# Kernel optimization log

Measured on AMD Instinct MI355X. Metric: run time of the kernel, lower is better.

## Reference

```python
import jax, jax.numpy as jnp
import numpy as np

N_HEADS = 8
D_MODEL = 512
HEAD_DIM = D_MODEL // N_HEADS


def setup_inputs() -> dict:
    key = jax.random.key(0)
    ks = jax.random.split(key, 9)
    B, T1, T2, D = 1, 4096, 4096, D_MODEL
    w_scale = 0.02
    return {
        "query": jax.random.normal(ks[0], (B, T1, D), dtype=jnp.float32),
        "key": jax.random.normal(ks[1], (B, T2, D), dtype=jnp.float32),
        "value": jax.random.normal(ks[2], (B, T2, D), dtype=jnp.float32),
        # True = padded (masked out); ~half positions masked
        "key_padding_mask": jax.random.randint(ks[3], (B, T2), 0, 2) == 1,
        "Wq_w": jax.random.normal(ks[4], (D, D), dtype=jnp.float32) * w_scale,
        "Wq_b": jnp.zeros((D,), dtype=jnp.float32),
        "Wk_w": jax.random.normal(ks[5], (D, D), dtype=jnp.float32) * w_scale,
        "Wk_b": jnp.zeros((D,), dtype=jnp.float32),
        "Wv_w": jax.random.normal(ks[6], (D, D), dtype=jnp.float32) * w_scale,
        "Wv_b": jnp.zeros((D,), dtype=jnp.float32),
        "Wo_w": jax.random.normal(ks[7], (D, D), dtype=jnp.float32) * w_scale,
        "Wo_b": jnp.zeros((D,), dtype=jnp.float32),
    }


def reference(query, key, value, key_padding_mask,
              Wq_w, Wq_b, Wk_w, Wk_b, Wv_w, Wv_b, Wo_w, Wo_b):
    B, T1, D = query.shape
    T2 = key.shape[1]
    H, HD = N_HEADS, HEAD_DIM

    # torch Linear: y = x @ W.T + b
    q = (query @ Wq_w.T + Wq_b).reshape(B, T1, H, HD).transpose(0, 2, 1, 3)  # [B,H,T1,HD]
    k = (key @ Wk_w.T + Wk_b).reshape(B, T2, H, HD).transpose(0, 2, 1, 3)    # [B,H,T2,HD]
    v = (value @ Wv_w.T + Wv_b).reshape(B, T2, H, HD).transpose(0, 2, 1, 3)  # [B,H,T2,HD]

    scale = 1.0 / (HD ** 0.5)
    scores = jnp.einsum("bhqd,bhkd->bhqk", q, k) * scale                     # [B,H,T1,T2]
    mask_value = jnp.finfo(scores.dtype).min
    scores = jnp.where(key_padding_mask[:, None, None, :], mask_value, scores)

    attn = jax.nn.softmax(scores, axis=-1)                                   # [B,H,T1,T2]
    # dropout p=0.0 (inference) -> identity

    out = jnp.einsum("bhqk,bhkd->bhqd", attn, v)                             # [B,H,T1,HD]
    out = out.transpose(0, 2, 1, 3).reshape(B, T1, D)
    out = out @ Wo_w.T + Wo_b
    return (out, attn)
```

## Files before the change

kernel.cpp:

```cpp
#include <hip/hip_runtime.h>
#include <hip/hip_bf16.h>
#include <float.h>
#include <stdint.h>

typedef __bf16 bf16x8 __attribute__((ext_vector_type(8)));
typedef __bf16 bf16x4 __attribute__((ext_vector_type(4)));
typedef float  f32x4  __attribute__((ext_vector_type(4)));

#define T_SEQ 4096
#define DMODEL 512
#define NH 8
#define HDIM 64
#define KS1 4
#define L2E 1.44269504088896340736f

__device__ __forceinline__ float fexp2(float x) { return __builtin_amdgcn_exp2f(x); }

__device__ __forceinline__ void gl_lds16(const __bf16* g, char* l) {
    __builtin_amdgcn_global_load_lds(
        (const __attribute__((address_space(1))) unsigned int*)(g),
        (__attribute__((address_space(3))) unsigned int*)(l),
        16, 0, 0);
}

__global__ __launch_bounds__(256) void qkv_kernel(
    const float* __restrict__ qin, const float* __restrict__ kin, const float* __restrict__ vin,
    const float* __restrict__ Wq, const float* __restrict__ bq,
    const float* __restrict__ Wk, const float* __restrict__ bk,
    const float* __restrict__ Wv, const float* __restrict__ bv,
    __bf16* __restrict__ qo, __bf16* __restrict__ ko, __bf16* __restrict__ vt)
{
    __shared__ char lds[16384];
    char* Ab = lds;
    char* Bb = lds + 8192;

    const int z = blockIdx.z;
    const float* X    = (z == 0) ? qin : (z == 1) ? kin : vin;
    const float* W    = (z == 0) ? Wq  : (z == 1) ? Wk  : Wv;
    const float* bias = (z == 0) ? bq  : (z == 1) ? bk  : bv;

    const int m0 = blockIdx.x * 64;
    const int n0 = blockIdx.y * 64;
    const int tid  = threadIdx.x;
    const int w    = tid >> 6;
    const int lane = tid & 63;
    const int lrow = lane & 15;
    const int lgrp = lane >> 4;

    f32x4 acc[4] = {};
    const int r  = tid >> 2;
    const int c0 = (tid & 3) * 16;

    for (int kt = 0; kt < 8; ++kt) {
        const int k0 = kt * 64;
        const float* gA = X + (size_t)(m0 + r) * DMODEL + k0 + c0;
        const float* gB = W + (size_t)(n0 + r) * DMODEL + k0 + c0;
        const int sw = (r & 7) << 4;
#pragma unroll
        for (int i = 0; i < 4; ++i) {
            float4 a4 = *(const float4*)(gA + 4 * i);
            float4 b4 = *(const float4*)(gB + 4 * i);
            bf16x4 av, bv4;
            av[0] = (__bf16)a4.x; av[1] = (__bf16)a4.y; av[2] = (__bf16)a4.z; av[3] = (__bf16)a4.w;
            bv4[0] = (__bf16)b4.x; bv4[1] = (__bf16)b4.y; bv4[2] = (__bf16)b4.z; bv4[3] = (__bf16)b4.w;
            *(bf16x4*)(Ab + r * 128 + ((c0 * 2 + 8 * i) ^ sw)) = av;
            *(bf16x4*)(Bb + r * 128 + ((c0 * 2 + 8 * i) ^ sw)) = bv4;
        }
        __syncthreads();
#pragma unroll
        for (int ks = 0; ks < 2; ++ks) {
            bf16x8 af = *(const bf16x8*)(Ab + (w * 16 + lrow) * 128 +
                                         ((ks * 64 + lgrp * 16) ^ ((lrow & 7) << 4)));
#pragma unroll
            for (int ns = 0; ns < 4; ++ns) {
                bf16x8 bf = *(const bf16x8*)(Bb + (ns * 16 + lrow) * 128 +
                                             ((ks * 64 + lgrp * 16) ^ ((lrow & 7) << 4)));
                acc[ns] = __builtin_amdgcn_mfma_f32_16x16x32_bf16(af, bf, acc[ns], 0, 0, 0);
            }
        }
        __syncthreads();
    }

    if (z == 2) {
        char* LT = lds;
#pragma unroll
        for (int ns = 0; ns < 4; ++ns) {
            float bcol = bias[n0 + ns * 16 + lrow];
#pragma unroll
            for (int rr = 0; rr < 4; ++rr) {
                int col = ns * 16 + lrow;
                int row = w * 16 + lgrp * 4 + rr;
                *(__bf16*)(LT + col * 128 + ((row * 2) ^ ((col & 7) << 4))) =
                    (__bf16)(acc[ns][rr] + bcol);
            }
        }
        __syncthreads();
        int d  = tid >> 2;
        int nb = (tid & 3) * 32;
        bf16x8 t0 = *(const bf16x8*)(LT + d * 128 + (nb ^ ((d & 7) << 4)));
        bf16x8 t1 = *(const bf16x8*)(LT + d * 128 + ((nb + 16) ^ ((d & 7) << 4)));
        __bf16* dst = vt + (size_t)(n0 + d) * T_SEQ + m0 + (tid & 3) * 16;
        *(bf16x8*)dst = t0;
        *(bf16x8*)(dst + 8) = t1;
    } else {
        __bf16* out = (z == 0) ? qo : ko;
        const float sc = (z == 0) ? 0.125f : 1.0f;
#pragma unroll
        for (int ns = 0; ns < 4; ++ns) {
            float bcol = bias[n0 + ns * 16 + lrow];
#pragma unroll
            for (int rr = 0; rr < 4; ++rr) {
                int orow = m0 + w * 16 + lgrp * 4 + rr;
                out[(size_t)orow * DMODEL + n0 + ns * 16 + lrow] =
                    (__bf16)((acc[ns][rr] + bcol) * sc);
            }
        }
    }
}

__global__ __launch_bounds__(256) void attn_stats(
    const __bf16* __restrict__ qb, const __bf16* __restrict__ kb,
    const int* __restrict__ mask, float* __restrict__ l_part)
{
    __shared__ char lds[16384];
    char* KB0 = lds;
    char* KB1 = lds + 8192;

    const int nwg  = 32 * NH * KS1;
    const int b    = blockIdx.x;
    const int rmap = (b & 7) * (nwg >> 3) + (b >> 3);
    const int qsi  = rmap & 31;
    const int h    = (rmap >> 5) & (NH - 1);
    const int ksp  = rmap >> 8;
    const int q0   = qsi * 128;
    const int k0   = ksp * (T_SEQ / KS1);

    const int tid  = threadIdx.x;
    const int w    = tid >> 6;
    const int lane = tid & 63;
    const int lrow = lane & 15;
    const int lgrp = lane >> 4;
    const int swl  = (lrow & 7) << 4;
    const int q0w  = q0 + w * 32;

    bf16x8 qa[2][2];
#pragma unroll
    for (int q2 = 0; q2 < 2; ++q2) {
        const __bf16* qp = qb + (size_t)(q0w + q2 * 16 + lrow) * DMODEL + h * HDIM;
        qa[q2][0] = *(const bf16x8*)(qp + lgrp * 8);
        qa[q2][1] = *(const bf16x8*)(qp + 32 + lgrp * 8);
    }

    const int key0 = w * 16 + (lane >> 3);
    const int key1 = key0 + 8;
    const int g    = lane & 7;
    const __bf16* sK0 = kb + (size_t)(k0 + key0) * DMODEL + h * HDIM + (g ^ (key0 & 7)) * 8;
    const __bf16* sK1 = kb + (size_t)(k0 + key1) * DMODEL + h * HDIM + (g ^ (key1 & 7)) * 8;

    float lsum[2][4] = {};

    gl_lds16(sK0, KB0 + w * 2048);
    gl_lds16(sK1, KB0 + w * 2048 + 1024);
    __syncthreads();

    char* cur = KB0;
    char* nxt = KB1;
    const int NT = (T_SEQ / KS1) / 64;
    for (int kt = 0; kt < NT; ++kt) {
        if (kt + 1 < NT) {
            gl_lds16(sK0 + (size_t)(kt + 1) * 64 * DMODEL, nxt + w * 2048);
            gl_lds16(sK1 + (size_t)(kt + 1) * 64 * DMODEL, nxt + w * 2048 + 1024);
        }

        f32x4 acc[2][4] = {};
        __builtin_amdgcn_s_setprio(1);
#pragma unroll
        for (int ns = 0; ns < 4; ++ns) {
            bf16x8 kf0 = *(const bf16x8*)(cur + (ns * 16 + lrow) * 128 + ((lgrp * 16) ^ swl));
            bf16x8 kf1 = *(const bf16x8*)(cur + (ns * 16 + lrow) * 128 + ((64 + lgrp * 16) ^ swl));
            acc[0][ns] = __builtin_amdgcn_mfma_f32_16x16x32_bf16(kf0, qa[0][0], acc[0][ns], 0, 0, 0);
            acc[0][ns] = __builtin_amdgcn_mfma_f32_16x16x32_bf16(kf1, qa[0][1], acc[0][ns], 0, 0, 0);
            acc[1][ns] = __builtin_amdgcn_mfma_f32_16x16x32_bf16(kf0, qa[1][0], acc[1][ns], 0, 0, 0);
            acc[1][ns] = __builtin_amdgcn_mfma_f32_16x16x32_bf16(kf1, qa[1][1], acc[1][ns], 0, 0, 0);
        }
        __builtin_amdgcn_s_setprio(0);

#pragma unroll
        for (int ns = 0; ns < 4; ++ns) {
            int4 mi = *(const int4*)(mask + k0 + kt * 64 + ns * 16 + lgrp * 4);
            f32x4 mb;
            mb[0] = mi.x ? -1e30f : 0.f;
            mb[1] = mi.y ? -1e30f : 0.f;
            mb[2] = mi.z ? -1e30f : 0.f;
            mb[3] = mi.w ? -1e30f : 0.f;
#pragma unroll
            for (int q2 = 0; q2 < 2; ++q2)
#pragma unroll
                for (int rr = 0; rr < 4; ++rr)
                    lsum[q2][ns] += fexp2(fmaf(acc[q2][ns][rr], L2E, mb[rr]));
        }
        __syncthreads();
        char* t = cur; cur = nxt; nxt = t;
    }

#pragma unroll
    for (int q2 = 0; q2 < 2; ++q2) {
        float tot = (lsum[q2][0] + lsum[q2][1]) + (lsum[q2][2] + lsum[q2][3]);
        tot += __shfl_xor(tot, 16);
        tot += __shfl_xor(tot, 32);
        if (lgrp == 0)
            l_part[((size_t)h * KS1 + ksp) * T_SEQ + q0w + q2 * 16 + lrow] = tot;
    }
}

__global__ __launch_bounds__(256) void attn_main(
    const __bf16* __restrict__ qb, const __bf16* __restrict__ kb,
    const __bf16* __restrict__ vt, const int* __restrict__ mask,
    const float* __restrict__ l_part,
    float* __restrict__ attn_out, void* __restrict__ opart,
    int KSP2, int of32)
{
    __shared__ char lds[40960];
    char* PB  = lds + 32768;

    const int nwg  = 64 * NH * KSP2;
    const int b    = blockIdx.x;
    const int rmap = (b & 7) * (nwg >> 3) + (b >> 3);
    const int qbi  = rmap & 63;
    const int h    = (rmap >> 6) & (NH - 1);
    const int kz   = rmap >> 9;
    const int q0   = qbi * 64;
    const int kspan = T_SEQ / KSP2;
    const int k0   = kz * kspan;
    const int NT   = kspan / 64;

    const int tid  = threadIdx.x;
    const int w    = tid >> 6;
    const int lane = tid & 63;
    const int lrow = lane & 15;
    const int lgrp = lane >> 4;
    const int swl  = (lrow & 7) << 4;

    bf16x8 qa[2];
    {
        const __bf16* qp = qb + (size_t)(q0 + w * 16 + lrow) * DMODEL + h * HDIM;
        qa[0] = *(const bf16x8*)(qp + lgrp * 8);
        qa[1] = *(const bf16x8*)(qp + 32 + lgrp * 8);
    }

    float rl;
    {
        float s = 0.f;
#pragma unroll
        for (int ks = 0; ks < KS1; ++ks)
            s += l_part[((size_t)h * KS1 + ks) * T_SEQ + q0 + w * 16 + lrow];
        rl = 1.0f / s;
    }

    const int key0 = w * 16 + (lane >> 3);
    const int key1 = key0 + 8;
    const int g    = lane & 7;
    const __bf16* sK0 = kb + (size_t)(k0 + key0) * DMODEL + h * HDIM + (g ^ (key0 & 7)) * 8;
    const __bf16* sK1 = kb + (size_t)(k0 + key1) * DMODEL + h * HDIM + (g ^ (key1 & 7)) * 8;
    const __bf16* sV0 = vt + (size_t)(h * HDIM + key0) * T_SEQ + k0 + (g ^ (key0 & 7)) * 8;
    const __bf16* sV1 = vt + (size_t)(h * HDIM + key1) * T_SEQ + k0 + (g ^ (key1 & 7)) * 8;

#define STAGE(tt, buf) do {                                             \
        size_t koff_ = (size_t)(tt) * 64 * DMODEL;                      \
        size_t voff_ = (size_t)(tt) * 64;                               \
        gl_lds16(sK0 + koff_, (buf) + w * 2048);                        \
        gl_lds16(sK1 + koff_, (buf) + w * 2048 + 1024);                 \
        gl_lds16(sV0 + voff_, (buf) + 8192 + w * 2048);                 \
        gl_lds16(sV1 + voff_, (buf) + 8192 + w * 2048 + 1024);          \
    } while (0)

    f32x4 oacc[4] = {};
    float* arow = attn_out + (size_t)h * T_SEQ * T_SEQ +
                  (size_t)(q0 + w * 16 + lrow) * T_SEQ + k0 + lgrp * 4;
    char* Pw = PB + w * 2048;

    char* bA = lds;
    char* bB = lds + 16384;

    STAGE(0, bA);
    __syncthreads();

    for (int kt = 0; kt < NT; ++kt) {
        if (kt + 1 < NT) STAGE(kt + 1, bB);

        f32x4 acc[4] = {};
        __builtin_amdgcn_s_setprio(1);
#pragma unroll
        for (int ns = 0; ns < 4; ++ns) {
            bf16x8 kf0 = *(const bf16x8*)(bA + (ns * 16 + lrow) * 128 + ((lgrp * 16) ^ swl));
            bf16x8 kf1 = *(const bf16x8*)(bA + (ns * 16 + lrow) * 128 + ((64 + lgrp * 16) ^ swl));
            acc[ns] = __builtin_amdgcn_mfma_f32_16x16x32_bf16(kf0, qa[0], acc[ns], 0, 0, 0);
            acc[ns] = __builtin_amdgcn_mfma_f32_16x16x32_bf16(kf1, qa[1], acc[ns], 0, 0, 0);
        }
        __builtin_amdgcn_s_setprio(0);

        f32x4 pvs[4];
#pragma unroll
        for (int ns = 0; ns < 4; ++ns) {
            int4 mi = *(const int4*)(mask + k0 + kt * 64 + ns * 16 + lgrp * 4);
            f32x4 mb;
            mb[0] = mi.x ? -1e30f : 0.f;
            mb[1] = mi.y ? -1e30f : 0.f;
            mb[2] = mi.z ? -1e30f : 0.f;
            mb[3] = mi.w ? -1e30f : 0.f;
            f32x4 pv;
#pragma unroll
            for (int rr = 0; rr < 4; ++rr)
                pv[rr] = fexp2(fmaf(acc[ns][rr], L2E, mb[rr])) * rl;
            pvs[ns] = pv;
            bf16x4 pb;
            pb[0] = (__bf16)pv[0]; pb[1] = (__bf16)pv[1];
            pb[2] = (__bf16)pv[2]; pb[3] = (__bf16)pv[3];
            *(bf16x4*)(Pw + lrow * 128 + ((ns * 32 + lgrp * 8) ^ swl)) = pb;
        }

        __builtin_amdgcn_s_setprio(1);
#pragma unroll
        for (int ks = 0; ks < 2; ++ks) {
            bf16x8 pa = *(const bf16x8*)(Pw + lrow * 128 + ((ks * 64 + lgrp * 16) ^ swl));
#pragma unroll
            for (int dsb = 0; dsb < 4; ++dsb) {
                bf16x8 vf = *(const bf16x8*)(bA + 8192 + (dsb * 16 + lrow) * 128 +
                                             ((ks * 64 + lgrp * 16) ^ swl));
                oacc[dsb] = __builtin_amdgcn_mfma_f32_16x16x32_bf16(vf, pa, oacc[dsb], 0, 0, 0);
            }
        }
        __builtin_amdgcn_s_setprio(0);

#pragma unroll
        for (int ns = 0; ns < 4; ++ns)
            *(f32x4*)(arow + kt * 64 + ns * 16) = pvs[ns];

        __syncthreads();
        char* tmp = bA; bA = bB; bB = tmp;
    }
#undef STAGE

    if (of32) {
        float* op = (float*)opart + (size_t)kz * T_SEQ * DMODEL +
                    (size_t)(q0 + w * 16 + lrow) * DMODEL + h * HDIM + lgrp * 4;
#pragma unroll
        for (int dsb = 0; dsb < 4; ++dsb)
            *(f32x4*)(op + dsb * 16) = oacc[dsb];
    } else {
        __bf16* op = (__bf16*)opart + (size_t)(q0 + w * 16 + lrow) * DMODEL + h * HDIM + lgrp * 4;
#pragma unroll
        for (int dsb = 0; dsb < 4; ++dsb) {
            bf16x4 ob;
            ob[0] = (__bf16)oacc[dsb][0]; ob[1] = (__bf16)oacc[dsb][1];
            ob[2] = (__bf16)oacc[dsb][2]; ob[3] = (__bf16)oacc[dsb][3];
            *(bf16x4*)(op + dsb * 16) = ob;
        }
    }
}

__global__ __launch_bounds__(256) void oproj_kernel(
    const void* __restrict__ opart, const float* __restrict__ Wo,
    const float* __restrict__ bo, float* __restrict__ out, int KSP2, int of32)
{
    __shared__ char lds[16384];
    char* Ab = lds;
    char* Bb = lds + 8192;

    const int m0 = blockIdx.x * 64;
    const int n0 = blockIdx.y * 64;
    const int tid  = threadIdx.x;
    const int w    = tid >> 6;
    const int lane = tid & 63;
    const int lrow = lane & 15;
    const int lgrp = lane >> 4;

    f32x4 acc[4] = {};
    const int r   = tid >> 2;
    const int c0e = (tid & 3) * 16;
    const int sw  = (r & 7) << 4;

    for (int kt = 0; kt < 8; ++kt) {
        const int k0 = kt * 64;
        if (of32) {
            const float* p0 = (const float*)opart + (size_t)(m0 + r) * DMODEL + k0 + c0e;
#pragma unroll
            for (int i = 0; i < 4; ++i) {
                f32x4 a4 = *(const f32x4*)(p0 + 4 * i);
                for (int s = 1; s < KSP2; ++s)
                    a4 = a4 + *(const f32x4*)(p0 + (size_t)s * T_SEQ * DMODEL + 4 * i);
                bf16x4 av;
                av[0] = (__bf16)a4[0]; av[1] = (__bf16)a4[1];
                av[2] = (__bf16)a4[2]; av[3] = (__bf16)a4[3];
                *(bf16x4*)(Ab + r * 128 + ((c0e * 2 + 8 * i) ^ sw)) = av;
            }
        } else {
            const __bf16* pa = (const __bf16*)opart + (size_t)(m0 + r) * DMODEL + k0 + c0e;
            bf16x8 a0 = *(const bf16x8*)pa;
            bf16x8 a1 = *(const bf16x8*)(pa + 8);
            *(bf16x8*)(Ab + r * 128 + ((c0e * 2) ^ sw)) = a0;
            *(bf16x8*)(Ab + r * 128 + ((c0e * 2 + 16) ^ sw)) = a1;
        }
        const float* gB = Wo + (size_t)(n0 + r) * DMODEL + k0 + c0e;
#pragma unroll
        for (int i = 0; i < 4; ++i) {
            float4 b4 = *(const float4*)(gB + 4 * i);
            bf16x4 bv4;
            bv4[0] = (__bf16)b4.x; bv4[1] = (__bf16)b4.y;
            bv4[2] = (__bf16)b4.z; bv4[3] = (__bf16)b4.w;
            *(bf16x4*)(Bb + r * 128 + ((c0e * 2 + 8 * i) ^ sw)) = bv4;
        }
        __syncthreads();
#pragma unroll
        for (int ks = 0; ks < 2; ++ks) {
            bf16x8 af = *(const bf16x8*)(Ab + (w * 16 + lrow) * 128 +
                                         ((ks * 64 + lgrp * 16) ^ ((lrow & 7) << 4)));
#pragma unroll
            for (int ns = 0; ns < 4; ++ns) {
                bf16x8 bf = *(const bf16x8*)(Bb + (ns * 16 + lrow) * 128 +
                                             ((ks * 64 + lgrp * 16) ^ ((lrow & 7) << 4)));
                acc[ns] = __builtin_amdgcn_mfma_f32_16x16x32_bf16(af, bf, acc[ns], 0, 0, 0);
            }
        }
        __syncthreads();
    }

#pragma unroll
    for (int ns = 0; ns < 4; ++ns) {
        float bcol = bo[n0 + ns * 16 + lrow];
#pragma unroll
        for (int rr = 0; rr < 4; ++rr) {
            int orow = m0 + w * 16 + lgrp * 4 + rr;
            out[(size_t)orow * DMODEL + n0 + ns * 16 + lrow] = acc[ns][rr] + bcol;
        }
    }
}

extern "C" void kernel_launch(void* const* d_in, const int* in_sizes, int n_in,
                              void* d_out, int out_size, void* d_ws, size_t ws_size,
                              hipStream_t stream) {
    const float* query = (const float*)d_in[0];
    const float* key   = (const float*)d_in[1];
    const float* value = (const float*)d_in[2];
    const int*   mask  = (const int*)d_in[3];
    const float* Wq = (const float*)d_in[4];
    const float* bq = (const float*)d_in[5];
    const float* Wk = (const float*)d_in[6];
    const float* bk = (const float*)d_in[7];
    const float* Wv = (const float*)d_in[8];
    const float* bv = (const float*)d_in[9];
    const float* Wo = (const float*)d_in[10];
    const float* bo = (const float*)d_in[11];

    float* out  = (float*)d_out;
    float* attn = out + (size_t)T_SEQ * DMODEL;

    char* ws = (char*)d_ws;
    __bf16* qo     = (__bf16*)(ws);
    __bf16* ko     = (__bf16*)(ws + (4u << 20));
    __bf16* vt     = (__bf16*)(ws + (8u << 20));
    float*  l_part = (float*)(ws + (12u << 20));
    void*   opart  = (void*)(ws + (12u << 20) + (1u << 19));
    const size_t obase = (12u << 20) + (1u << 19);

    int KSP2, of32;
    const size_t oslice = (size_t)T_SEQ * DMODEL * 4;
    if (ws_size >= obase + 2 * oslice)      { KSP2 = 2; of32 = 1; }
    else if (ws_size >= obase + oslice)     { KSP2 = 1; of32 = 1; }
    else                                    { KSP2 = 1; of32 = 0; }

    qkv_kernel<<<dim3(64, 8, 3), 256, 0, stream>>>(query, key, value,
                                                   Wq, bq, Wk, bk, Wv, bv, qo, ko, vt);
    attn_stats<<<dim3(32 * NH * KS1), 256, 0, stream>>>(qo, ko, mask, l_part);
    attn_main<<<dim3(64 * NH * KSP2), 256, 0, stream>>>(qo, ko, vt, mask, l_part,
                                                        attn, opart, KSP2, of32);
    oproj_kernel<<<dim3(64, 8), 256, 0, stream>>>(opart, Wo, bo, out, KSP2, of32);
}
```

Before: 233.5 us.

## Load V fragments directly from global into registers instead of via LDS

Removes V staging through LDS: each wave now loads its V^T MFMA fragments directly from global memory into registers, in two halves issued before and after the QK MFMAs. LDS shrinks from 40KB to 24KB, which may raise occupancy, and the attention-probability stores move into the softmax loop to save registers. The cost is that all four waves now redundantly fetch the same V tile from global or L2 with no cross-wave sharing, and the load latency is no longer hidden by the async double-buffered prefetch.

After: 288.7 us. 1.24x slower.

```diff
diff --git a/kernel.cpp b/kernel.cpp
--- a/kernel.cpp
+++ b/kernel.cpp
@@ -220,8 +220,8 @@
     float* __restrict__ attn_out, void* __restrict__ opart,
     int KSP2, int of32)
 {
-    __shared__ char lds[40960];
-    char* PB  = lds + 32768;
+    __shared__ char lds[24576];
+    char* PB  = lds + 16384;
 
     const int nwg  = 64 * NH * KSP2;
     const int b    = blockIdx.x;
@@ -262,16 +262,13 @@
     const int g    = lane & 7;
     const __bf16* sK0 = kb + (size_t)(k0 + key0) * DMODEL + h * HDIM + (g ^ (key0 & 7)) * 8;
     const __bf16* sK1 = kb + (size_t)(k0 + key1) * DMODEL + h * HDIM + (g ^ (key1 & 7)) * 8;
-    const __bf16* sV0 = vt + (size_t)(h * HDIM + key0) * T_SEQ + k0 + (g ^ (key0 & 7)) * 8;
-    const __bf16* sV1 = vt + (size_t)(h * HDIM + key1) * T_SEQ + k0 + (g ^ (key1 & 7)) * 8;
+
+    const __bf16* vbase = vt + (size_t)(h * HDIM + lrow) * T_SEQ + k0 + lgrp * 8;
 
 #define STAGE(tt, buf) do {                                             \
         size_t koff_ = (size_t)(tt) * 64 * DMODEL;                      \
-        size_t voff_ = (size_t)(tt) * 64;                               \
         gl_lds16(sK0 + koff_, (buf) + w * 2048);                        \
         gl_lds16(sK1 + koff_, (buf) + w * 2048 + 1024);                 \
-        gl_lds16(sV0 + voff_, (buf) + 8192 + w * 2048);                 \
-        gl_lds16(sV1 + voff_, (buf) + 8192 + w * 2048 + 1024);          \
     } while (0)
 
     f32x4 oacc[4] = {};
@@ -280,13 +277,19 @@
     char* Pw = PB + w * 2048;
 
     char* bA = lds;
-    char* bB = lds + 16384;
+    char* bB = lds + 8192;
 
     STAGE(0, bA);
     __syncthreads();
 
     for (int kt = 0; kt < NT; ++kt) {
         if (kt + 1 < NT) STAGE(kt + 1, bB);
+
+        const __bf16* vpt = vbase + (size_t)kt * 64;
+        bf16x8 vf0[4];
+#pragma unroll
+        for (int dsb = 0; dsb < 4; ++dsb)
+            vf0[dsb] = *(const bf16x8*)(vpt + (size_t)(dsb * 16) * T_SEQ);
 
         f32x4 acc[4] = {};
         __builtin_amdgcn_s_setprio(1);
@@ -299,7 +302,11 @@
         }
         __builtin_amdgcn_s_setprio(0);
 
-        f32x4 pvs[4];
+        bf16x8 vf1[4];
+#pragma unroll
+        for (int dsb = 0; dsb < 4; ++dsb)
+            vf1[dsb] = *(const bf16x8*)(vpt + (size_t)(dsb * 16) * T_SEQ + 32);
+
 #pragma unroll
         for (int ns = 0; ns < 4; ++ns) {
             int4 mi = *(const int4*)(mask + k0 + kt * 64 + ns * 16 + lgrp * 4);
@@ -312,29 +319,25 @@
 #pragma unroll
             for (int rr = 0; rr < 4; ++rr)
                 pv[rr] = fexp2(fmaf(acc[ns][rr], L2E, mb[rr])) * rl;
-            pvs[ns] = pv;
             bf16x4 pb;
             pb[0] = (__bf16)pv[0]; pb[1] = (__bf16)pv[1];
             pb[2] = (__bf16)pv[2]; pb[3] = (__bf16)pv[3];
             *(bf16x4*)(Pw + lrow * 128 + ((ns * 32 + lgrp * 8) ^ swl)) = pb;
+            *(f32x4*)(arow + kt * 64 + ns * 16) = pv;
         }
 
         __builtin_amdgcn_s_setprio(1);
-#pragma unroll
-        for (int ks = 0; ks < 2; ++ks) {
-            bf16x8 pa = *(const bf16x8*)(Pw + lrow * 128 + ((ks * 64 + lgrp * 16) ^ swl));
-#pragma unroll
-            for (int dsb = 0; dsb < 4; ++dsb) {
-                bf16x8 vf = *(const bf16x8*)(bA + 8192 + (dsb * 16 + lrow) * 128 +
-                                             ((ks * 64 + lgrp * 16) ^ swl));
-                oacc[dsb] = __builtin_amdgcn_mfma_f32_16x16x32_bf16(vf, pa, oacc[dsb], 0, 0, 0);
-            }
+        {
+            bf16x8 pa0 = *(const bf16x8*)(Pw + lrow * 128 + ((lgrp * 16) ^ swl));
+#pragma unroll
+            for (int dsb = 0; dsb < 4; ++dsb)
+                oacc[dsb] = __builtin_amdgcn_mfma_f32_16x16x32_bf16(vf0[dsb], pa0, oacc[dsb], 0, 0, 0);
+            bf16x8 pa1 = *(const bf16x8*)(Pw + lrow * 128 + ((64 + lgrp * 16) ^ swl));
+#pragma unroll
+            for (int dsb = 0; dsb < 4; ++dsb)
+                oacc[dsb] = __builtin_amdgcn_mfma_f32_16x16x32_bf16(vf1[dsb], pa1, oacc[dsb], 0, 0, 0);
         }
         __builtin_amdgcn_s_setprio(0);
-
-#pragma unroll
-        for (int ns = 0; ns < 4; ++ns)
-            *(f32x4*)(arow + kt * 64 + ns * 16) = pvs[ns];
 
         __syncthreads();
         char* tmp = bA; bA = bB; bB = tmp;
```
